# Kernel tuning notes

Measured on AMD Instinct MI355X. Metric: run time of the kernel, lower is better.

## Reference

```python
import jax, jax.numpy as jnp
import numpy as np

EPS = 1e-5

def rotate_half(x):
    # interleaved pairs: (..., d*2) -> stack(-x2, x1) interleaved back
    x = x.reshape(*x.shape[:-1], -1, 2)
    x1, x2 = x[..., 0], x[..., 1]
    return jnp.stack((-x2, x1), axis=-1).reshape(*x.shape[:-2], -1)

def apply_rotary(freqs, x):
    # freqs: (b, n, d); x: (b, h, n, d) -> broadcast over heads (unsqueeze at dim=1)
    f = freqs[:, None, :, :]
    return x * jnp.cos(f) + rotate_half(x) * jnp.sin(f)

def layer_norm(x, g, b):
    mu = jnp.mean(x, axis=-1, keepdims=True)
    var = jnp.var(x, axis=-1, keepdims=True)
    return (x - mu) * jax.lax.rsqrt(var + EPS) * g + b

def setup_inputs() -> dict:
    key = jax.random.key(0)
    ks = jax.random.split(key, 10)
    b, nq, nkv, dim, h, dh = 8, 1024, 2048, 512, 8, 64
    inner = h * dh
    return {
        "x_query": jax.random.normal(ks[0], (b, nq, dim), jnp.float32),
        "x_context": jax.random.normal(ks[1], (b, nkv, dim), jnp.float32),
        "rotary_time_emb_query": jax.random.normal(ks[2], (b, nq, dh), jnp.float32),
        "rotary_time_emb_context": jax.random.normal(ks[3], (b, nkv, dh), jnp.float32),
        "context_mask": jnp.ones((b, nkv), dtype=bool),
        "ln_q_g": jnp.ones((dim,), jnp.float32),
        "ln_q_b": jnp.zeros((dim,), jnp.float32),
        "ln_c_g": jnp.ones((dim,), jnp.float32),
        "ln_c_b": jnp.zeros((dim,), jnp.float32),
        "Wq": jax.random.normal(ks[4], (dim, inner), jnp.float32) * 0.02,
        "Wkv": jax.random.normal(ks[5], (dim, 2 * inner), jnp.float32) * 0.02,
        "Wo": jax.random.normal(ks[6], (inner, dim), jnp.float32) * 0.02,
        "bo": jnp.zeros((dim,), jnp.float32),
    }

def reference(x_query, x_context, rotary_time_emb_query, rotary_time_emb_context,
              context_mask, ln_q_g, ln_q_b, ln_c_g, ln_c_b, Wq, Wkv, Wo, bo):
    h = 8
    xq = layer_norm(x_query, ln_q_g, ln_q_b)
    xc = layer_norm(x_context, ln_c_g, ln_c_b)
    q = xq @ Wq                       # (b, nq, inner)
    kv = xc @ Wkv                     # (b, nkv, 2*inner)
    k, v = jnp.split(kv, 2, axis=-1)
    split_heads = lambda t: t.reshape(t.shape[0], t.shape[1], h, -1).transpose(0, 2, 1, 3)
    q, k, v = split_heads(q), split_heads(k), split_heads(v)  # (b, h, n, dh)
    q = apply_rotary(rotary_time_emb_query, q)
    k = apply_rotary(rotary_time_emb_context, k)
    v = apply_rotary(rotary_time_emb_context, v)   # rotate_value=True
    dh = q.shape[-1]
    scale = 1.0 / jnp.sqrt(jnp.float32(dh))
    scores = jnp.einsum('bhqd,bhkd->bhqk', q, k) * scale
    neg = jnp.finfo(scores.dtype).min
    scores = jnp.where(context_mask[:, None, None, :], scores, neg)
    attn = jax.nn.softmax(scores, axis=-1)
    out = jnp.einsum('bhqk,bhkd->bhqd', attn, v)
    out = apply_rotary(-rotary_time_emb_query, out)  # inverse rotation
    out = out.transpose(0, 2, 1, 3).reshape(out.shape[0], out.shape[2], -1)  # (b, nq, inner)
    return out @ Wo + bo
```

## Files before the change

kernel.cpp:

```cpp
#include <hip/hip_runtime.h>
#include <hip/hip_bf16.h>
#include <math.h>

#define BB 8
#define NQ 1024
#define NKV 2048
#define DIM 512
#define H 8
#define DH 64
#define INNER 512
#define SCALE_LOG2E 0.18033688011112042f

typedef __bf16 bf16x8 __attribute__((ext_vector_type(8)));
typedef float f32x4 __attribute__((ext_vector_type(4)));
typedef unsigned int u32x4 __attribute__((ext_vector_type(4)));

__device__ __forceinline__ unsigned short f2bf(float f) {
  union { float f; unsigned int u; } v; v.f = f;
  unsigned int r = v.u + 0x7fffu + ((v.u >> 16) & 1u);
  return (unsigned short)(r >> 16);
}
__device__ __forceinline__ float bf2f(unsigned short h) {
  union { unsigned int u; float f; } v; v.u = ((unsigned int)h) << 16;
  return v.f;
}

__device__ __forceinline__ void gl_lds16(const unsigned short* g, unsigned short* l) {
  __builtin_amdgcn_global_load_lds(
      (const __attribute__((address_space(1))) unsigned int*)g,
      (__attribute__((address_space(3))) unsigned int*)l, 16, 0, 0);
}

__global__ __launch_bounds__(256) void prep_weights(
    const float* __restrict__ Wq, const float* __restrict__ Wkv,
    const float* __restrict__ Wo,
    unsigned short* __restrict__ WqT, unsigned short* __restrict__ WkvT,
    unsigned short* __restrict__ WohT, unsigned short* __restrict__ WolT) {
  __shared__ float T[64][65];
  int blk = blockIdx.x;
  const float* src; int Wd, ti, tj, mode;
  unsigned short* dst = nullptr;
  if (blk < 64) { src = Wq;  dst = WqT;  Wd = 512;  ti = blk >> 3; tj = blk & 7; mode = 0; }
  else if (blk < 192) { int b2 = blk - 64; src = Wkv; dst = WkvT; Wd = 1024; ti = b2 >> 4; tj = b2 & 15; mode = 0; }
  else { int b2 = blk - 192; src = Wo; Wd = 512; ti = b2 >> 3; tj = b2 & 7; mode = 1; }
  int t = threadIdx.x;
#pragma unroll
  for (int i = 0; i < 16; ++i) {
    int idx = i * 256 + t;
    int r = idx >> 6, c = idx & 63;
    T[r][c] = src[(size_t)(ti * 64 + r) * Wd + tj * 64 + c];
  }
  __syncthreads();
#pragma unroll
  for (int i = 0; i < 16; ++i) {
    int idx = i * 256 + t;
    int n = idx >> 6, k = idx & 63;
    float v = T[k][n];
    size_t off = (size_t)(tj * 64 + n) * 512 + ti * 64 + k;
    if (mode == 0) {
      dst[off] = f2bf(v);
    } else {
      unsigned short hb = f2bf(v);
      WohT[off] = hb;
      WolT[off] = f2bf(v - bf2f(hb));
    }
  }
}

__global__ __launch_bounds__(256) void ln_kernel(
    const float* __restrict__ xq, const float* __restrict__ xc,
    const float* __restrict__ gq, const float* __restrict__ bq,
    const float* __restrict__ gc, const float* __restrict__ bc,
    unsigned short* __restrict__ xq_bf, unsigned short* __restrict__ xc_bf) {
  int row = blockIdx.x;
  const float* x; const float* g; const float* bb; unsigned short* out;
  if (row < BB * NQ) {
    x = xq + (size_t)row * DIM; g = gq; bb = bq; out = xq_bf + (size_t)row * DIM;
  } else {
    int r = row - BB * NQ;
    x = xc + (size_t)r * DIM; g = gc; bb = bc; out = xc_bf + (size_t)r * DIM;
  }
  int t = threadIdx.x;
  float2 v = *reinterpret_cast<const float2*>(x + t * 2);
  float s = v.x + v.y;
  float ss = v.x * v.x + v.y * v.y;
#pragma unroll
  for (int d = 1; d < 64; d <<= 1) { s += __shfl_xor(s, d); ss += __shfl_xor(ss, d); }
  __shared__ float red[8];
  int wid = t >> 6, lane = t & 63;
  if (lane == 0) { red[wid] = s; red[4 + wid] = ss; }
  __syncthreads();
  s = red[0] + red[1] + red[2] + red[3];
  ss = red[4] + red[5] + red[6] + red[7];
  float mu = s * (1.0f / DIM);
  float var = ss * (1.0f / DIM) - mu * mu;
  float rs = rsqrtf(var + 1e-5f);
  float y0 = (v.x - mu) * rs * g[t * 2] + bb[t * 2];
  float y1 = (v.y - mu) * rs * g[t * 2 + 1] + bb[t * 2 + 1];
  ushort2 o; o.x = f2bf(y0); o.y = f2bf(y1);
  *reinterpret_cast<ushort2*>(out + t * 2) = o;
}

__device__ __forceinline__ void gemm128_mainloop(
    const unsigned short* __restrict__ A, const unsigned short* __restrict__ WT,
    unsigned short* As, unsigned short* Ws,
    int rowBase, int colBase, f32x4 acc[4][4]) {
  const int t = threadIdx.x;
  const int w = t >> 6, l = t & 63;
  const int l15 = l & 15, lg = l >> 4, c7 = l15 & 7;
  const int wr = w >> 1, wc = w & 1;
  const int lrow = l >> 3;
  const int lchunk = (l & 7) ^ lrow;
  const int frag = (lg ^ c7) * 8;
  const unsigned short* Ag = A + (size_t)rowBase * 512;
  const unsigned short* Wg = WT + (size_t)colBase * 512;
#pragma unroll
  for (int m = 0; m < 4; ++m)
#pragma unroll
    for (int n = 0; n < 4; ++n) acc[m][n] = f32x4{0.f, 0.f, 0.f, 0.f};
  for (int kb = 0; kb < 512; kb += 64) {
#pragma unroll
    for (int i = 0; i < 4; ++i) {
      const int seg = w * 4 + i;
      const size_t goff = (size_t)(seg * 8 + lrow) * 512 + kb + lchunk * 8;
      gl_lds16(Ag + goff, As + seg * 512);
      gl_lds16(Wg + goff, Ws + seg * 512);
    }
    __syncthreads();
#pragma unroll
    for (int ks = 0; ks < 2; ++ks) {
      const int xo = ks ? 32 : 0;
      bf16x8 af[4], bf_[4];
#pragma unroll
      for (int m = 0; m < 4; ++m)
        af[m] = *reinterpret_cast<const bf16x8*>(
            &As[(wr * 64 + m * 16 + l15) * 64 + (frag ^ xo)]);
#pragma unroll
      for (int n = 0; n < 4; ++n)
        bf_[n] = *reinterpret_cast<const bf16x8*>(
            &Ws[(wc * 64 + n * 16 + l15) * 64 + (frag ^ xo)]);
#pragma unroll
      for (int m = 0; m < 4; ++m)
#pragma unroll
        for (int n = 0; n < 4; ++n)
          acc[m][n] = __builtin_amdgcn_mfma_f32_16x16x32_bf16(af[m], bf_[n], acc[m][n], 0, 0, 0);
    }
    __syncthreads();
  }
}

__global__ __launch_bounds__(256) void proj_q(
    const unsigned short* __restrict__ xq_bf, const unsigned short* __restrict__ WqT,
    const float* __restrict__ rotq, unsigned short* __restrict__ Qb) {
  __shared__ __align__(16) char smem[128 * 66 * 4];
  unsigned short* As = (unsigned short*)smem;
  unsigned short* Ws = (unsigned short*)(smem + 16384);
  float (*Cs)[66] = (float(*)[66])smem;
  int o = blockIdx.x;
  int swz = ((o & 7) << 5) | (o >> 3);
  int bn = swz & 3, bm = swz >> 2;
  f32x4 acc[4][4];
  gemm128_mainloop(xq_bf, WqT, As, Ws, bm * 128, bn * 128, acc);
  const int t = threadIdx.x;
  const int w = t >> 6, l = t & 63;
  const int l15 = l & 15, lg = l >> 4;
  const int wr = w >> 1, wc = w & 1;
#pragma unroll
  for (int hc = 0; hc < 2; ++hc) {
    if (wc == hc) {
#pragma unroll
      for (int m = 0; m < 4; ++m)
#pragma unroll
        for (int n = 0; n < 4; ++n)
#pragma unroll
          for (int r = 0; r < 4; ++r)
            Cs[wr * 64 + m * 16 + lg * 4 + r][n * 16 + l15] = acc[m][n][r];
    }
    __syncthreads();
    const int head = bn * 2 + hc;
#pragma unroll
    for (int i = 0; i < 16; ++i) {
      int p = i * 256 + t;
      int row = p >> 5, pc = p & 31, d0 = pc * 2;
      int grow = bm * 128 + row;
      float c0 = Cs[row][d0], c1 = Cs[row][d0 + 1];
      const float* f = rotq + (size_t)grow * DH + d0;
      float f0 = f[0], f1 = f[1], s0, s1, co0, co1;
      __sincosf(f0, &s0, &co0);
      __sincosf(f1, &s1, &co1);
      float o0 = (c0 * co0 - c1 * s0) * SCALE_LOG2E;
      float o1 = (c1 * co1 + c0 * s1) * SCALE_LOG2E;
      ushort2 ov; ov.x = f2bf(o0); ov.y = f2bf(o1);
      int b = grow >> 10, qq = grow & 1023;
      *reinterpret_cast<ushort2*>(Qb + (((size_t)(b * H + head) * NQ + qq) * DH + d0)) = ov;
    }
    __syncthreads();
  }
}

__global__ __launch_bounds__(256) void proj_kv(
    const unsigned short* __restrict__ xc_bf, const unsigned short* __restrict__ WkvT,
    const float* __restrict__ rotc, const int* __restrict__ cmask,
    unsigned short* __restrict__ Kb, unsigned short* __restrict__ VTb) {
  __shared__ __align__(16) char smem[128 * 66 * 4];
  unsigned short* As = (unsigned short*)smem;
  unsigned short* Ws = (unsigned short*)(smem + 16384);
  float (*Cs)[66] = (float(*)[66])smem;
  int o = blockIdx.x;
  int swz = ((o & 7) << 7) | (o >> 3);
  int bn = swz & 7, bm = swz >> 3;
  f32x4 acc[4][4];
  gemm128_mainloop(xc_bf, WkvT, As, Ws, bm * 128, bn * 128, acc);
  const int t = threadIdx.x;
  const int w = t >> 6, l = t & 63;
  const int l15 = l & 15, lg = l >> 4;
  const int wr = w >> 1, wc = w & 1;
#pragma unroll
  for (int hc = 0; hc < 2; ++hc) {
    if (wc == hc) {
#pragma unroll
      for (int m = 0; m < 4; ++m)
#pragma unroll
        for (int n = 0; n < 4; ++n)
#pragma unroll
          for (int r = 0; r < 4; ++r)
            Cs[wr * 64 + m * 16 + lg * 4 + r][n * 16 + l15] = acc[m][n][r];
    }
    __syncthreads();
    const int g = bn * 2 + hc;
    const int h = g & 7;
    if (g < 8) {
#pragma unroll
      for (int i = 0; i < 16; ++i) {
        int p = i * 256 + t;
        int row = p >> 5, pc = p & 31, d0 = pc * 2;
        int grow = bm * 128 + row;
        float c0 = Cs[row][d0], c1 = Cs[row][d0 + 1];
        const float* f = rotc + (size_t)grow * DH + d0;
        float f0 = f[0], f1 = f[1], s0, s1, co0, co1;
        __sincosf(f0, &s0, &co0);
        __sincosf(f1, &s1, &co1);
        float mf = cmask[grow] ? 1.f : 0.f;
        float o0 = (c0 * co0 - c1 * s0) * mf;
        float o1 = (c1 * co1 + c0 * s1) * mf;
        int b = grow >> 11, kk = grow & 2047;
        ushort2 ov; ov.x = f2bf(o0); ov.y = f2bf(o1);
        *reinterpret_cast<ushort2*>(Kb + (((size_t)(b * H + h) * NKV + kk) * DH + d0)) = ov;
      }
    } else {
      int oc = t & 7;
      int dd0 = t >> 3;
#pragma unroll
      for (int ch = 0; ch < 2; ++ch) {
        int ch64 = bm * 2 + ch;
        int bb = ch64 >> 5, chunk = ch64 & 31;
        unsigned short* vbase = VTb + (((size_t)(bb * H + h) * 32 + chunk) * 64) * 64;
#pragma unroll
        for (int half = 0; half < 2; ++half) {
          int d = dd0 + half * 32;
          u32x4 pack;
#pragma unroll
          for (int j2 = 0; j2 < 4; ++j2) {
            unsigned int lohi[2];
#pragma unroll
            for (int e = 0; e < 2; ++e) {
              int p = oc * 8 + j2 * 2 + e;
              int pp = p & 31;
              int kv = (p >> 5) * 32 + ((pp & 1) ? ((pp >> 1) + 16) : (pp >> 1));
              float c0 = Cs[ch * 64 + kv][d], cx = Cs[ch * 64 + kv][d ^ 1];
              float f = rotc[(size_t)(ch64 * 64 + kv) * DH + d];
              float sn, cs;
              __sincosf(f, &sn, &cs);
              float mf = cmask[ch64 * 64 + kv] ? 1.f : 0.f;
              float val = ((d & 1) ? (c0 * cs + cx * sn) : (c0 * cs - cx * sn)) * mf;
              lohi[e] = f2bf(val);
            }
            pack[j2] = lohi[0] | (lohi[1] << 16);
          }
          *reinterpret_cast<u32x4*>(vbase + d * 64 + oc * 8) = pack;
        }
      }
    }
    __syncthreads();
  }
}

__global__ __launch_bounds__(256) void attn_kernel(
    const unsigned short* __restrict__ Qb, const unsigned short* __restrict__ Kb,
    const unsigned short* __restrict__ VTb, const int* __restrict__ mask,
    const float* __restrict__ rotq,
    unsigned short* __restrict__ Ahb, unsigned short* __restrict__ Alb) {
  __shared__ unsigned short Ks[2 * 64 * 64];
  __shared__ unsigned short Vs[2 * 64 * 64];
  __shared__ unsigned short Ps[4 * 16 * 64];
  int ob = blockIdx.x;
  int swz = ((ob & 7) << 7) + (ob >> 3);
  int qb = swz & 15;
  int bh = swz >> 4;
  int b = bh >> 3, hh = bh & 7;
  int t = threadIdx.x, w = t >> 6, l = t & 63;
  int l15 = l & 15, lg = l >> 4;
  int c7 = l15 & 7;

  float nmasked;
  {
    const int* mrow = mask + b * NKV;
    float msum = 0.f;
#pragma unroll
    for (int i = 0; i < 8; ++i) {
      int4 m = *reinterpret_cast<const int4*>(mrow + l * 4 + i * 256);
      msum += (m.x ? 1.f : 0.f) + (m.y ? 1.f : 0.f) +
              (m.z ? 1.f : 0.f) + (m.w ? 1.f : 0.f);
    }
#pragma unroll
    for (int d = 1; d < 64; d <<= 1) msum += __shfl_xor(msum, d);
    nmasked = (float)NKV - msum;
  }

  const unsigned short* qrow = Qb + ((size_t)bh * NQ + qb * 64 + w * 16 + l15) * DH;
  bf16x8 qa0 = *reinterpret_cast<const bf16x8*>(qrow + lg * 8);
  bf16x8 qa1 = *reinterpret_cast<const bf16x8*>(qrow + 32 + lg * 8);

  float plsum[4] = {0.f, 0.f, 0.f, 0.f};
  f32x4 acc[4];
#pragma unroll
  for (int ct = 0; ct < 4; ++ct) acc[ct] = f32x4{0.f, 0.f, 0.f, 0.f};

  const int srow = t >> 2;
  const int sseg = (t & 3) * 16;
  const int sdst0 = srow * 64 + ((2 * (t & 3)) ^ (srow & 7)) * 8;
  const int frag = (lg ^ c7) * 8;
  const int kbase = l15 * 64 + frag;
  const int prbase = w * 1024 + l15 * 64 + frag;
  unsigned int* pw = reinterpret_cast<unsigned int*>(Ps);
  const int lg4 = lg * 4, l3 = l15 & 3, sD = l15 >> 2;

  const unsigned short* gk = Kb + ((size_t)bh * NKV + srow) * DH + sseg;
  const unsigned short* gv = VTb + (((size_t)bh * 32) * 64 + srow) * 64 + sseg;

  bf16x8 kr0 = *reinterpret_cast<const bf16x8*>(gk);
  bf16x8 kr1 = *reinterpret_cast<const bf16x8*>(gk + 8);
  bf16x8 vr0 = *reinterpret_cast<const bf16x8*>(gv);
  bf16x8 vr1 = *reinterpret_cast<const bf16x8*>(gv + 8);
  gk += 4096; gv += 4096;

#pragma unroll 2
  for (int ic = 0; ic < NKV / 64; ++ic) {
    const int bo_ = (ic & 1) << 12;
    *reinterpret_cast<bf16x8*>(&Ks[bo_ + sdst0])       = kr0;
    *reinterpret_cast<bf16x8*>(&Ks[bo_ + (sdst0 ^ 8)]) = kr1;
    *reinterpret_cast<bf16x8*>(&Vs[bo_ + sdst0])       = vr0;
    *reinterpret_cast<bf16x8*>(&Vs[bo_ + (sdst0 ^ 8)]) = vr1;
    __syncthreads();
    if (ic + 1 < NKV / 64) {
      kr0 = *reinterpret_cast<const bf16x8*>(gk);
      kr1 = *reinterpret_cast<const bf16x8*>(gk + 8);
      vr0 = *reinterpret_cast<const bf16x8*>(gv);
      vr1 = *reinterpret_cast<const bf16x8*>(gv + 8);
      gk += 4096; gv += 4096;
    }
    f32x4 s[4];
    __builtin_amdgcn_s_setprio(1);
#pragma unroll
    for (int tt = 0; tt < 4; ++tt) {
      f32x4 z = f32x4{0.f, 0.f, 0.f, 0.f};
      bf16x8 k0 = *reinterpret_cast<const bf16x8*>(&Ks[bo_ + tt * 1024 + kbase]);
      z = __builtin_amdgcn_mfma_f32_16x16x32_bf16(qa0, k0, z, 0, 0, 0);
      bf16x8 k1 = *reinterpret_cast<const bf16x8*>(&Ks[bo_ + tt * 1024 + (kbase ^ 32)]);
      z = __builtin_amdgcn_mfma_f32_16x16x32_bf16(qa1, k1, z, 0, 0, 0);
      s[tt] = z;
    }
    __builtin_amdgcn_s_setprio(0);
    float p[4][4];
#pragma unroll
    for (int tt = 0; tt < 4; ++tt)
#pragma unroll
      for (int r = 0; r < 4; ++r) {
        float e;
        asm("v_exp_f32 %0, %1" : "=v"(e) : "v"(s[tt][r]));
        p[tt][r] = e;
      }
#pragma unroll
    for (int r = 0; r < 4; ++r)
      plsum[r] += (p[0][r] + p[1][r]) + (p[2][r] + p[3][r]);
#pragma unroll
    for (int r = 0; r < 4; ++r) {
      unsigned int d01, d23;
      asm("v_cvt_pk_bf16_f32 %0, %1, %2" : "=v"(d01) : "v"(p[0][r]), "v"(p[1][r]));
      asm("v_cvt_pk_bf16_f32 %0, %1, %2" : "=v"(d23) : "v"(p[2][r]), "v"(p[3][r]));
      int row = lg4 + r;
      int rb = row & 7;
      int dwl = ((sD ^ rb) << 2) + l3;
      int pb = w * 512 + row * 32 + dwl;
      pw[pb] = d01;
      pw[pb ^ 16] = d23;
    }
    asm volatile("s_waitcnt lgkmcnt(0)" ::: "memory");
    __builtin_amdgcn_sched_barrier(0);
    __builtin_amdgcn_s_setprio(1);
#pragma unroll
    for (int ks = 0; ks < 2; ++ks) {
      bf16x8 pa = *reinterpret_cast<const bf16x8*>(&Ps[(prbase ^ (ks ? 32 : 0))]);
#pragma unroll
      for (int ct = 0; ct < 4; ++ct) {
        bf16x8 vb = *reinterpret_cast<const bf16x8*>(
            &Vs[bo_ + ct * 1024 + (kbase ^ (ks ? 32 : 0))]);
        acc[ct] = __builtin_amdgcn_mfma_f32_16x16x32_bf16(pa, vb, acc[ct], 0, 0, 0);
      }
    }
    __builtin_amdgcn_s_setprio(0);
  }
#pragma unroll
  for (int d = 1; d < 16; d <<= 1)
#pragma unroll
    for (int r = 0; r < 4; ++r) plsum[r] += __shfl_xor(plsum[r], d);
  float inv[4];
#pragma unroll
  for (int r = 0; r < 4; ++r) inv[r] = 1.0f / (plsum[r] - nmasked);

  int q0 = qb * 64 + w * 16 + lg * 4;
#pragma unroll
  for (int r = 0; r < 4; ++r) {
    int grow = b * NQ + q0 + r;
    const float* frow = rotq + (size_t)grow * DH;
    size_t obase = (size_t)grow * INNER + hh * DH;
#pragma unroll
    for (int ct = 0; ct < 4; ++ct) {
      int d = ct * 16 + l15;
      float x = acc[ct][r] * inv[r];
      float nb = __shfl_xor(x, 1);
      float f = frow[d];
      float sn, cs;
      __sincosf(f, &sn, &cs);
      float ov = (d & 1) ? (x * cs - nb * sn) : (x * cs + nb * sn);
      unsigned short hb = f2bf(ov);
      Ahb[obase + d] = hb;
      Alb[obase + d] = f2bf(ov - bf2f(hb));
    }
  }
}

__global__ __launch_bounds__(256) void final_gemm(
    const unsigned short* __restrict__ Ah, const unsigned short* __restrict__ Al,
    const unsigned short* __restrict__ Wh, const unsigned short* __restrict__ Wl,
    const float* __restrict__ bo, float* __restrict__ out) {
  __shared__ __align__(16) char smem[65536];
  unsigned short* AhS = (unsigned short*)smem;
  unsigned short* AlS = (unsigned short*)(smem + 16384);
  unsigned short* WhS = (unsigned short*)(smem + 32768);
  unsigned short* WlS = (unsigned short*)(smem + 49152);
  int o = blockIdx.x;
  int swz = ((o & 7) << 5) | (o >> 3);
  int bn = swz & 3, bm = swz >> 2;
  const int t = threadIdx.x;
  const int w = t >> 6, l = t & 63;
  const int l15 = l & 15, lg = l >> 4, c7 = l15 & 7;
  const int wr = w >> 1, wc = w & 1;
  const int lrow = l >> 3;
  const int lchunk = (l & 7) ^ lrow;
  const int frag = (lg ^ c7) * 8;
  const unsigned short* Agh = Ah + (size_t)bm * 128 * 512;
  const unsigned short* Agl = Al + (size_t)bm * 128 * 512;
  const unsigned short* Wgh = Wh + (size_t)bn * 128 * 512;
  const unsigned short* Wgl = Wl + (size_t)bn * 128 * 512;
  f32x4 acc[4][4];
#pragma unroll
  for (int m = 0; m < 4; ++m)
#pragma unroll
    for (int n = 0; n < 4; ++n) acc[m][n] = f32x4{0.f, 0.f, 0.f, 0.f};
  for (int kb = 0; kb < 512; kb += 64) {
#pragma unroll
    for (int i = 0; i < 4; ++i) {
      const int seg = w * 4 + i;
      const size_t goff = (size_t)(seg * 8 + lrow) * 512 + kb + lchunk * 8;
      gl_lds16(Agh + goff, AhS + seg * 512);
      gl_lds16(Agl + goff, AlS + seg * 512);
      gl_lds16(Wgh + goff, WhS + seg * 512);
      gl_lds16(Wgl + goff, WlS + seg * 512);
    }
    __syncthreads();
#pragma unroll
    for (int ks = 0; ks < 2; ++ks) {
      const int xo = ks ? 32 : 0;
      bf16x8 ah[4], al[4], wh[4], wl[4];
#pragma unroll
      for (int m = 0; m < 4; ++m) {
        const int off = (wr * 64 + m * 16 + l15) * 64 + (frag ^ xo);
        ah[m] = *reinterpret_cast<const bf16x8*>(&AhS[off]);
        al[m] = *reinterpret_cast<const bf16x8*>(&AlS[off]);
      }
#pragma unroll
      for (int n = 0; n < 4; ++n) {
        const int off = (wc * 64 + n * 16 + l15) * 64 + (frag ^ xo);
        wh[n] = *reinterpret_cast<const bf16x8*>(&WhS[off]);
        wl[n] = *reinterpret_cast<const bf16x8*>(&WlS[off]);
      }
#pragma unroll
      for (int m = 0; m < 4; ++m)
#pragma unroll
        for (int n = 0; n < 4; ++n) {
          acc[m][n] = __builtin_amdgcn_mfma_f32_16x16x32_bf16(ah[m], wh[n], acc[m][n], 0, 0, 0);
          acc[m][n] = __builtin_amdgcn_mfma_f32_16x16x32_bf16(al[m], wh[n], acc[m][n], 0, 0, 0);
          acc[m][n] = __builtin_amdgcn_mfma_f32_16x16x32_bf16(ah[m], wl[n], acc[m][n], 0, 0, 0);
        }
    }
    __syncthreads();
  }
  const int row0 = bm * 128 + wr * 64;
  const int col0 = bn * 128 + wc * 64;
#pragma unroll
  for (int m = 0; m < 4; ++m)
#pragma unroll
    for (int n = 0; n < 4; ++n) {
      int col = col0 + n * 16 + l15;
      float bv = bo[col];
#pragma unroll
      for (int r = 0; r < 4; ++r)
        out[(size_t)(row0 + m * 16 + lg * 4 + r) * 512 + col] = acc[m][n][r] + bv;
    }
}

extern "C" void kernel_launch(void* const* d_in, const int* in_sizes, int n_in,
                              void* d_out, int out_size, void* d_ws, size_t ws_size,
                              hipStream_t stream) {
  const float* x_query   = (const float*)d_in[0];
  const float* x_context = (const float*)d_in[1];
  const float* rot_q     = (const float*)d_in[2];
  const float* rot_c     = (const float*)d_in[3];
  const int*   cmask     = (const int*)d_in[4];
  const float* ln_q_g    = (const float*)d_in[5];
  const float* ln_q_b    = (const float*)d_in[6];
  const float* ln_c_g    = (const float*)d_in[7];
  const float* ln_c_b    = (const float*)d_in[8];
  const float* Wq        = (const float*)d_in[9];
  const float* Wkv       = (const float*)d_in[10];
  const float* Wo        = (const float*)d_in[11];
  const float* bo        = (const float*)d_in[12];
  float* out = (float*)d_out;

  char* ws = (char*)d_ws;
  unsigned short* xq_bf = (unsigned short*)(ws + 0);
  unsigned short* xc_bf = (unsigned short*)(ws + 8388608);
  unsigned short* Ahb   = (unsigned short*)(ws + 0);
  unsigned short* Alb   = (unsigned short*)(ws + 8388608);
  unsigned short* WqT   = (unsigned short*)(ws + 25165824);
  unsigned short* WkvT  = (unsigned short*)(ws + 25690112);
  unsigned short* Qb    = (unsigned short*)(ws + 26738688);
  unsigned short* Kb    = (unsigned short*)(ws + 35127296);
  unsigned short* VTb   = (unsigned short*)(ws + 51904512);
  unsigned short* WohT  = (unsigned short*)(ws + 68681728);
  unsigned short* WolT  = (unsigned short*)(ws + 69206016);

  prep_weights<<<dim3(256), dim3(256), 0, stream>>>(Wq, Wkv, Wo, WqT, WkvT, WohT, WolT);
  ln_kernel<<<dim3(24576), dim3(256), 0, stream>>>(x_query, x_context, ln_q_g, ln_q_b,
                                                   ln_c_g, ln_c_b, xq_bf, xc_bf);
  proj_q<<<dim3(256), dim3(256), 0, stream>>>(xq_bf, WqT, rot_q, Qb);
  proj_kv<<<dim3(1024), dim3(256), 0, stream>>>(xc_bf, WkvT, rot_c, cmask, Kb, VTb);
  attn_kernel<<<dim3(1024), dim3(256), 0, stream>>>(Qb, Kb, VTb, cmask, rot_q, Ahb, Alb);
  final_gemm<<<dim3(256), dim3(256), 0, stream>>>(Ahb, Alb, WohT, WolT, bo, out);
}
```

Baseline: 158.3 us.

## Merge prep and layernorm launches, fuse Q/KV projections, shrink final GEMM tile

Weight preparation and layernorm now run in one kernel, with each layernorm block handling 12 rows. The Q and KV projection kernels are merged into a single launch that branches on block index. The final output GEMM tile shrinks from 128x128 to 128x64, doubling the grid to 512 blocks and reducing LDS use. The aim is to cut launch count and tail idle time and to raise occupancy, at the cost of more redundant A-tile loads in the final GEMM and an extra barrier per layernorm row.

```diff
diff --git a/kernel.cpp b/kernel.cpp
--- a/kernel.cpp
+++ b/kernel.cpp
@@ -31,74 +31,77 @@
       (__attribute__((address_space(3))) unsigned int*)l, 16, 0, 0);
 }
 
-__global__ __launch_bounds__(256) void prep_weights(
+__global__ __launch_bounds__(256) void prep_ln(
     const float* __restrict__ Wq, const float* __restrict__ Wkv,
     const float* __restrict__ Wo,
     unsigned short* __restrict__ WqT, unsigned short* __restrict__ WkvT,
-    unsigned short* __restrict__ WohT, unsigned short* __restrict__ WolT) {
-  __shared__ float T[64][65];
-  int blk = blockIdx.x;
-  const float* src; int Wd, ti, tj, mode;
-  unsigned short* dst = nullptr;
-  if (blk < 64) { src = Wq;  dst = WqT;  Wd = 512;  ti = blk >> 3; tj = blk & 7; mode = 0; }
-  else if (blk < 192) { int b2 = blk - 64; src = Wkv; dst = WkvT; Wd = 1024; ti = b2 >> 4; tj = b2 & 15; mode = 0; }
-  else { int b2 = blk - 192; src = Wo; Wd = 512; ti = b2 >> 3; tj = b2 & 7; mode = 1; }
-  int t = threadIdx.x;
-#pragma unroll
-  for (int i = 0; i < 16; ++i) {
-    int idx = i * 256 + t;
-    int r = idx >> 6, c = idx & 63;
-    T[r][c] = src[(size_t)(ti * 64 + r) * Wd + tj * 64 + c];
-  }
-  __syncthreads();
-#pragma unroll
-  for (int i = 0; i < 16; ++i) {
-    int idx = i * 256 + t;
-    int n = idx >> 6, k = idx & 63;
-    float v = T[k][n];
-    size_t off = (size_t)(tj * 64 + n) * 512 + ti * 64 + k;
-    if (mode == 0) {
-      dst[off] = f2bf(v);
-    } else {
-      unsigned short hb = f2bf(v);
-      WohT[off] = hb;
-      WolT[off] = f2bf(v - bf2f(hb));
-    }
-  }
-}
-
-__global__ __launch_bounds__(256) void ln_kernel(
+    unsigned short* __restrict__ WohT, unsigned short* __restrict__ WolT,
     const float* __restrict__ xq, const float* __restrict__ xc,
     const float* __restrict__ gq, const float* __restrict__ bq,
     const float* __restrict__ gc, const float* __restrict__ bc,
     unsigned short* __restrict__ xq_bf, unsigned short* __restrict__ xc_bf) {
-  int row = blockIdx.x;
-  const float* x; const float* g; const float* bb; unsigned short* out;
-  if (row < BB * NQ) {
-    x = xq + (size_t)row * DIM; g = gq; bb = bq; out = xq_bf + (size_t)row * DIM;
+  __shared__ float T[64][65];
+  __shared__ float red[8];
+  int blk = blockIdx.x;
+  int t = threadIdx.x;
+  if (blk < 2048) {
+    int wid = t >> 6, lane = t & 63;
+    for (int rr = 0; rr < 12; ++rr) {
+      int row = blk * 12 + rr;
+      const float* x; const float* g; const float* bbv; unsigned short* outp;
+      if (row < BB * NQ) {
+        x = xq + (size_t)row * DIM; g = gq; bbv = bq; outp = xq_bf + (size_t)row * DIM;
+      } else {
+        int r2 = row - BB * NQ;
+        x = xc + (size_t)r2 * DIM; g = gc; bbv = bc; outp = xc_bf + (size_t)r2 * DIM;
+      }
+      float2 v = *reinterpret_cast<const float2*>(x + t * 2);
+      float s = v.x + v.y;
+      float ss = v.x * v.x + v.y * v.y;
+#pragma unroll
+      for (int d = 1; d < 64; d <<= 1) { s += __shfl_xor(s, d); ss += __shfl_xor(ss, d); }
+      if (lane == 0) { red[wid] = s; red[4 + wid] = ss; }
+      __syncthreads();
+      s = red[0] + red[1] + red[2] + red[3];
+      ss = red[4] + red[5] + red[6] + red[7];
+      __syncthreads();
+      float mu = s * (1.0f / DIM);
+      float var = ss * (1.0f / DIM) - mu * mu;
+      float rs = rsqrtf(var + 1e-5f);
+      float y0 = (v.x - mu) * rs * g[t * 2] + bbv[t * 2];
+      float y1 = (v.y - mu) * rs * g[t * 2 + 1] + bbv[t * 2 + 1];
+      ushort2 o; o.x = f2bf(y0); o.y = f2bf(y1);
+      *reinterpret_cast<ushort2*>(outp + t * 2) = o;
+    }
   } else {
-    int r = row - BB * NQ;
-    x = xc + (size_t)r * DIM; g = gc; bb = bc; out = xc_bf + (size_t)r * DIM;
-  }
-  int t = threadIdx.x;
-  float2 v = *reinterpret_cast<const float2*>(x + t * 2);
-  float s = v.x + v.y;
-  float ss = v.x * v.x + v.y * v.y;
-#pragma unroll
-  for (int d = 1; d < 64; d <<= 1) { s += __shfl_xor(s, d); ss += __shfl_xor(ss, d); }
-  __shared__ float red[8];
-  int wid = t >> 6, lane = t & 63;
-  if (lane == 0) { red[wid] = s; red[4 + wid] = ss; }
-  __syncthreads();
-  s = red[0] + red[1] + red[2] + red[3];
-  ss = red[4] + red[5] + red[6] + red[7];
-  float mu = s * (1.0f / DIM);
-  float var = ss * (1.0f / DIM) - mu * mu;
-  float rs = rsqrtf(var + 1e-5f);
-  float y0 = (v.x - mu) * rs * g[t * 2] + bb[t * 2];
-  float y1 = (v.y - mu) * rs * g[t * 2 + 1] + bb[t * 2 + 1];
-  ushort2 o; o.x = f2bf(y0); o.y = f2bf(y1);
-  *reinterpret_cast<ushort2*>(out + t * 2) = o;
+    int blk2 = blk - 2048;
+    const float* src; int Wd, ti, tj, mode;
+    unsigned short* dst = nullptr;
+    if (blk2 < 64) { src = Wq;  dst = WqT;  Wd = 512;  ti = blk2 >> 3; tj = blk2 & 7; mode = 0; }
+    else if (blk2 < 192) { int b2 = blk2 - 64; src = Wkv; dst = WkvT; Wd = 1024; ti = b2 >> 4; tj = b2 & 15; mode = 0; }
+    else { int b2 = blk2 - 192; src = Wo; Wd = 512; ti = b2 >> 3; tj = b2 & 7; mode = 1; }
+#pragma unroll
+    for (int i = 0; i < 16; ++i) {
+      int idx = i * 256 + t;
+      int r = idx >> 6, c = idx & 63;
+      T[r][c] = src[(size_t)(ti * 64 + r) * Wd + tj * 64 + c];
+    }
+    __syncthreads();
+#pragma unroll
+    for (int i = 0; i < 16; ++i) {
+      int idx = i * 256 + t;
+      int n = idx >> 6, k = idx & 63;
+      float v = T[k][n];
+      size_t off = (size_t)(tj * 64 + n) * 512 + ti * 64 + k;
+      if (mode == 0) {
+        dst[off] = f2bf(v);
+      } else {
+        unsigned short hb = f2bf(v);
+        WohT[off] = hb;
+        WolT[off] = f2bf(v - bf2f(hb));
+      }
+    }
+  }
 }
 
 __device__ __forceinline__ void gemm128_mainloop(
@@ -149,139 +152,131 @@
   }
 }
 
-__global__ __launch_bounds__(256) void proj_q(
-    const unsigned short* __restrict__ xq_bf, const unsigned short* __restrict__ WqT,
-    const float* __restrict__ rotq, unsigned short* __restrict__ Qb) {
+__global__ __launch_bounds__(256) void proj_fused(
+    const unsigned short* __restrict__ xq_bf, const unsigned short* __restrict__ xc_bf,
+    const unsigned short* __restrict__ WqT, const unsigned short* __restrict__ WkvT,
+    const float* __restrict__ rotq, const float* __restrict__ rotc,
+    const int* __restrict__ cmask,
+    unsigned short* __restrict__ Qb, unsigned short* __restrict__ Kb,
+    unsigned short* __restrict__ VTb) {
   __shared__ __align__(16) char smem[128 * 66 * 4];
   unsigned short* As = (unsigned short*)smem;
   unsigned short* Ws = (unsigned short*)(smem + 16384);
   float (*Cs)[66] = (float(*)[66])smem;
-  int o = blockIdx.x;
-  int swz = ((o & 7) << 5) | (o >> 3);
-  int bn = swz & 3, bm = swz >> 2;
-  f32x4 acc[4][4];
-  gemm128_mainloop(xq_bf, WqT, As, Ws, bm * 128, bn * 128, acc);
   const int t = threadIdx.x;
   const int w = t >> 6, l = t & 63;
   const int l15 = l & 15, lg = l >> 4;
   const int wr = w >> 1, wc = w & 1;
-#pragma unroll
-  for (int hc = 0; hc < 2; ++hc) {
-    if (wc == hc) {
-#pragma unroll
-      for (int m = 0; m < 4; ++m)
-#pragma unroll
-        for (int n = 0; n < 4; ++n)
-#pragma unroll
-          for (int r = 0; r < 4; ++r)
-            Cs[wr * 64 + m * 16 + lg * 4 + r][n * 16 + l15] = acc[m][n][r];
-    }
-    __syncthreads();
-    const int head = bn * 2 + hc;
-#pragma unroll
-    for (int i = 0; i < 16; ++i) {
-      int p = i * 256 + t;
-      int row = p >> 5, pc = p & 31, d0 = pc * 2;
-      int grow = bm * 128 + row;
-      float c0 = Cs[row][d0], c1 = Cs[row][d0 + 1];
-      const float* f = rotq + (size_t)grow * DH + d0;
-      float f0 = f[0], f1 = f[1], s0, s1, co0, co1;
-      __sincosf(f0, &s0, &co0);
-      __sincosf(f1, &s1, &co1);
-      float o0 = (c0 * co0 - c1 * s0) * SCALE_LOG2E;
-      float o1 = (c1 * co1 + c0 * s1) * SCALE_LOG2E;
-      ushort2 ov; ov.x = f2bf(o0); ov.y = f2bf(o1);
-      int b = grow >> 10, qq = grow & 1023;
-      *reinterpret_cast<ushort2*>(Qb + (((size_t)(b * H + head) * NQ + qq) * DH + d0)) = ov;
-    }
-    __syncthreads();
-  }
-}
-
-__global__ __launch_bounds__(256) void proj_kv(
-    const unsigned short* __restrict__ xc_bf, const unsigned short* __restrict__ WkvT,
-    const float* __restrict__ rotc, const int* __restrict__ cmask,
-    unsigned short* __restrict__ Kb, unsigned short* __restrict__ VTb) {
-  __shared__ __align__(16) char smem[128 * 66 * 4];
-  unsigned short* As = (unsigned short*)smem;
-  unsigned short* Ws = (unsigned short*)(smem + 16384);
-  float (*Cs)[66] = (float(*)[66])smem;
+  f32x4 acc[4][4];
   int o = blockIdx.x;
-  int swz = ((o & 7) << 7) | (o >> 3);
-  int bn = swz & 7, bm = swz >> 3;
-  f32x4 acc[4][4];
-  gemm128_mainloop(xc_bf, WkvT, As, Ws, bm * 128, bn * 128, acc);
-  const int t = threadIdx.x;
-  const int w = t >> 6, l = t & 63;
-  const int l15 = l & 15, lg = l >> 4;
-  const int wr = w >> 1, wc = w & 1;
-#pragma unroll
-  for (int hc = 0; hc < 2; ++hc) {
-    if (wc == hc) {
-#pragma unroll
-      for (int m = 0; m < 4; ++m)
-#pragma unroll
-        for (int n = 0; n < 4; ++n)
-#pragma unroll
-          for (int r = 0; r < 4; ++r)
-            Cs[wr * 64 + m * 16 + lg * 4 + r][n * 16 + l15] = acc[m][n][r];
-    }
-    __syncthreads();
-    const int g = bn * 2 + hc;
-    const int h = g & 7;
-    if (g < 8) {
+  if (o < 1024) {
+    int swz = ((o & 7) << 7) | (o >> 3);
+    int bn = swz & 7, bm = swz >> 3;
+    gemm128_mainloop(xc_bf, WkvT, As, Ws, bm * 128, bn * 128, acc);
+#pragma unroll
+    for (int hc = 0; hc < 2; ++hc) {
+      if (wc == hc) {
+#pragma unroll
+        for (int m = 0; m < 4; ++m)
+#pragma unroll
+          for (int n = 0; n < 4; ++n)
+#pragma unroll
+            for (int r = 0; r < 4; ++r)
+              Cs[wr * 64 + m * 16 + lg * 4 + r][n * 16 + l15] = acc[m][n][r];
+      }
+      __syncthreads();
+      const int g = bn * 2 + hc;
+      const int h = g & 7;
+      if (g < 8) {
+#pragma unroll
+        for (int i = 0; i < 16; ++i) {
+          int p = i * 256 + t;
+          int row = p >> 5, pc = p & 31, d0 = pc * 2;
+          int grow = bm * 128 + row;
+          float c0 = Cs[row][d0], c1 = Cs[row][d0 + 1];
+          const float* f = rotc + (size_t)grow * DH + d0;
+          float f0 = f[0], f1 = f[1], s0, s1, co0, co1;
+          __sincosf(f0, &s0, &co0);
+          __sincosf(f1, &s1, &co1);
+          float mf = cmask[grow] ? 1.f : 0.f;
+          float o0 = (c0 * co0 - c1 * s0) * mf;
+          float o1 = (c1 * co1 + c0 * s1) * mf;
+          int b = grow >> 11, kk = grow & 2047;
+          ushort2 ov; ov.x = f2bf(o0); ov.y = f2bf(o1);
+          *reinterpret_cast<ushort2*>(Kb + (((size_t)(b * H + h) * NKV + kk) * DH + d0)) = ov;
+        }
+      } else {
+        int oc = t & 7;
+        int dd0 = t >> 3;
+#pragma unroll
+        for (int ch = 0; ch < 2; ++ch) {
+          int ch64 = bm * 2 + ch;
+          int bb = ch64 >> 5, chunk = ch64 & 31;
+          unsigned short* vbase = VTb + (((size_t)(bb * H + h) * 32 + chunk) * 64) * 64;
+#pragma unroll
+          for (int half = 0; half < 2; ++half) {
+            int d = dd0 + half * 32;
+            u32x4 pack;
+#pragma unroll
+            for (int j2 = 0; j2 < 4; ++j2) {
+              unsigned int lohi[2];
+#pragma unroll
+              for (int e = 0; e < 2; ++e) {
+                int p = oc * 8 + j2 * 2 + e;
+                int pp = p & 31;
+                int kv = (p >> 5) * 32 + ((pp & 1) ? ((pp >> 1) + 16) : (pp >> 1));
+                float c0 = Cs[ch * 64 + kv][d], cx = Cs[ch * 64 + kv][d ^ 1];
+                float f = rotc[(size_t)(ch64 * 64 + kv) * DH + d];
+                float sn, cs;
+                __sincosf(f, &sn, &cs);
+                float mf = cmask[ch64 * 64 + kv] ? 1.f : 0.f;
+                float val = ((d & 1) ? (c0 * cs + cx * sn) : (c0 * cs - cx * sn)) * mf;
+                lohi[e] = f2bf(val);
+              }
+              pack[j2] = lohi[0] | (lohi[1] << 16);
+            }
+            *reinterpret_cast<u32x4*>(vbase + d * 64 + oc * 8) = pack;
+          }
+        }
+      }
+      __syncthreads();
+    }
+  } else {
+    int o2 = o - 1024;
+    int swz = ((o2 & 7) << 5) | (o2 >> 3);
+    int bn = swz & 3, bm = swz >> 2;
+    gemm128_mainloop(xq_bf, WqT, As, Ws, bm * 128, bn * 128, acc);
+#pragma unroll
+    for (int hc = 0; hc < 2; ++hc) {
+      if (wc == hc) {
+#pragma unroll
+        for (int m = 0; m < 4; ++m)
+#pragma unroll
+          for (int n = 0; n < 4; ++n)
+#pragma unroll
+            for (int r = 0; r < 4; ++r)
+              Cs[wr * 64 + m * 16 + lg * 4 + r][n * 16 + l15] = acc[m][n][r];
+      }
+      __syncthreads();
+      const int head = bn * 2 + hc;
 #pragma unroll
       for (int i = 0; i < 16; ++i) {
         int p = i * 256 + t;
         int row = p >> 5, pc = p & 31, d0 = pc * 2;
         int grow = bm * 128 + row;
         float c0 = Cs[row][d0], c1 = Cs[row][d0 + 1];
-        const float* f = rotc + (size_t)grow * DH + d0;
+        const float* f = rotq + (size_t)grow * DH + d0;
         float f0 = f[0], f1 = f[1], s0, s1, co0, co1;
         __sincosf(f0, &s0, &co0);
         __sincosf(f1, &s1, &co1);
-        float mf = cmask[grow] ? 1.f : 0.f;
-        float o0 = (c0 * co0 - c1 * s0) * mf;
-        float o1 = (c1 * co1 + c0 * s1) * mf;
-        int b = grow >> 11, kk = grow & 2047;
+        float o0 = (c0 * co0 - c1 * s0) * SCALE_LOG2E;
+        float o1 = (c1 * co1 + c0 * s1) * SCALE_LOG2E;
         ushort2 ov; ov.x = f2bf(o0); ov.y = f2bf(o1);
-        *reinterpret_cast<ushort2*>(Kb + (((size_t)(b * H + h) * NKV + kk) * DH + d0)) = ov;
-      }
-    } else {
-      int oc = t & 7;
-      int dd0 = t >> 3;
-#pragma unroll
-      for (int ch = 0; ch < 2; ++ch) {
-        int ch64 = bm * 2 + ch;
-        int bb = ch64 >> 5, chunk = ch64 & 31;
-        unsigned short* vbase = VTb + (((size_t)(bb * H + h) * 32 + chunk) * 64) * 64;
-#pragma unroll
-        for (int half = 0; half < 2; ++half) {
-          int d = dd0 + half * 32;
-          u32x4 pack;
-#pragma unroll
-          for (int j2 = 0; j2 < 4; ++j2) {
-            unsigned int lohi[2];
-#pragma unroll
-            for (int e = 0; e < 2; ++e) {
-              int p = oc * 8 + j2 * 2 + e;
-              int pp = p & 31;
-              int kv = (p >> 5) * 32 + ((pp & 1) ? ((pp >> 1) + 16) : (pp >> 1));
-              float c0 = Cs[ch * 64 + kv][d], cx = Cs[ch * 64 + kv][d ^ 1];
-              float f = rotc[(size_t)(ch64 * 64 + kv) * DH + d];
-              float sn, cs;
-              __sincosf(f, &sn, &cs);
-              float mf = cmask[ch64 * 64 + kv] ? 1.f : 0.f;
-              float val = ((d & 1) ? (c0 * cs + cx * sn) : (c0 * cs - cx * sn)) * mf;
-              lohi[e] = f2bf(val);
-            }
-            pack[j2] = lohi[0] | (lohi[1] << 16);
-          }
-          *reinterpret_cast<u32x4*>(vbase + d * 64 + oc * 8) = pack;
-        }
-      }
-    }
-    __syncthreads();
+        int b = grow >> 10, qq = grow & 1023;
+        *reinterpret_cast<ushort2*>(Qb + (((size_t)(b * H + head) * NQ + qq) * DH + d0)) = ov;
+      }
+      __syncthreads();
+    }
   }
 }
 
@@ -444,14 +439,14 @@
     const unsigned short* __restrict__ Ah, const unsigned short* __restrict__ Al,
     const unsigned short* __restrict__ Wh, const unsigned short* __restrict__ Wl,
     const float* __restrict__ bo, float* __restrict__ out) {
-  __shared__ __align__(16) char smem[65536];
+  __shared__ __align__(16) char smem[49152];
   unsigned short* AhS = (unsigned short*)smem;
   unsigned short* AlS = (unsigned short*)(smem + 16384);
   unsigned short* WhS = (unsigned short*)(smem + 32768);
-  unsigned short* WlS = (unsigned short*)(smem + 49152);
+  unsigned short* WlS = (unsigned short*)(smem + 40960);
   int o = blockIdx.x;
-  int swz = ((o & 7) << 5) | (o >> 3);
-  int bn = swz & 3, bm = swz >> 2;
+  int swz = ((o & 7) << 6) | (o >> 3);
+  int bn = swz & 7, bm = swz >> 3;
   const int t = threadIdx.x;
   const int w = t >> 6, l = t & 63;
   const int l15 = l & 15, lg = l >> 4, c7 = l15 & 7;
@@ -461,13 +456,13 @@
   const int frag = (lg ^ c7) * 8;
   const unsigned short* Agh = Ah + (size_t)bm * 128 * 512;
   const unsigned short* Agl = Al + (size_t)bm * 128 * 512;
-  const unsigned short* Wgh = Wh + (size_t)bn * 128 * 512;
-  const unsigned short* Wgl = Wl + (size_t)bn * 128 * 512;
-  f32x4 acc[4][4];
+  const unsigned short* Wgh = Wh + (size_t)bn * 64 * 512;
+  const unsigned short* Wgl = Wl + (size_t)bn * 64 * 512;
+  f32x4 acc[4][2];
 #pragma unroll
   for (int m = 0; m < 4; ++m)
 #pragma unroll
-    for (int n = 0; n < 4; ++n) acc[m][n] = f32x4{0.f, 0.f, 0.f, 0.f};
+    for (int n = 0; n < 2; ++n) acc[m][n] = f32x4{0.f, 0.f, 0.f, 0.f};
   for (int kb = 0; kb < 512; kb += 64) {
 #pragma unroll
     for (int i = 0; i < 4; ++i) {
@@ -475,6 +470,11 @@
       const size_t goff = (size_t)(seg * 8 + lrow) * 512 + kb + lchunk * 8;
       gl_lds16(Agh + goff, AhS + seg * 512);
       gl_lds16(Agl + goff, AlS + seg * 512);
+    }
+#pragma unroll
+    for (int i = 0; i < 2; ++i) {
+      const int seg = w * 2 + i;
+      const size_t goff = (size_t)(seg * 8 + lrow) * 512 + kb + lchunk * 8;
       gl_lds16(Wgh + goff, WhS + seg * 512);
       gl_lds16(Wgl + goff, WlS + seg * 512);
     }
@@ -482,7 +482,7 @@
 #pragma unroll
     for (int ks = 0; ks < 2; ++ks) {
       const int xo = ks ? 32 : 0;
-      bf16x8 ah[4], al[4], wh[4], wl[4];
+      bf16x8 ah[4], al[4], wh[2], wl[2];
 #pragma unroll
       for (int m = 0; m < 4; ++m) {
         const int off = (wr * 64 + m * 16 + l15) * 64 + (frag ^ xo);
@@ -490,15 +490,15 @@
         al[m] = *reinterpret_cast<const bf16x8*>(&AlS[off]);
       }
 #pragma unroll
-      for (int n = 0; n < 4; ++n) {
-        const int off = (wc * 64 + n * 16 + l15) * 64 + (frag ^ xo);
+      for (int n = 0; n < 2; ++n) {
+        const int off = (wc * 32 + n * 16 + l15) * 64 + (frag ^ xo);
         wh[n] = *reinterpret_cast<const bf16x8*>(&WhS[off]);
         wl[n] = *reinterpret_cast<const bf16x8*>(&WlS[off]);
       }
 #pragma unroll
       for (int m = 0; m < 4; ++m)
 #pragma unroll
-        for (int n = 0; n < 4; ++n) {
+        for (int n = 0; n < 2; ++n) {
           acc[m][n] = __builtin_amdgcn_mfma_f32_16x16x32_bf16(ah[m], wh[n], acc[m][n], 0, 0, 0);
           acc[m][n] = __builtin_amdgcn_mfma_f32_16x16x32_bf16(al[m], wh[n], acc[m][n], 0, 0, 0);
           acc[m][n] = __builtin_amdgcn_mfma_f32_16x16x32_bf16(ah[m], wl[n], acc[m][n], 0, 0, 0);
@@ -507,11 +507,11 @@
     __syncthreads();
   }
   const int row0 = bm * 128 + wr * 64;
-  const int col0 = bn * 128 + wc * 64;
+  const int col0 = bn * 64 + wc * 32;
 #pragma unroll
   for (int m = 0; m < 4; ++m)
 #pragma unroll
-    for (int n = 0; n < 4; ++n) {
+    for (int n = 0; n < 2; ++n) {
       int col = col0 + n * 16 + l15;
       float bv = bo[col];
 #pragma unroll
@@ -551,11 +551,11 @@
   unsigned short* WohT  = (unsigned short*)(ws + 68681728);
   unsigned short* WolT  = (unsigned short*)(ws + 69206016);
 
-  prep_weights<<<dim3(256), dim3(256), 0, stream>>>(Wq, Wkv, Wo, WqT, WkvT, WohT, WolT);
-  ln_kernel<<<dim3(24576), dim3(256), 0, stream>>>(x_query, x_context, ln_q_g, ln_q_b,
-                                                   ln_c_g, ln_c_b, xq_bf, xc_bf);
-  proj_q<<<dim3(256), dim3(256), 0, stream>>>(xq_bf, WqT, rot_q, Qb);
-  proj_kv<<<dim3(1024), dim3(256), 0, stream>>>(xc_bf, WkvT, rot_c, cmask, Kb, VTb);
+  prep_ln<<<dim3(2304), dim3(256), 0, stream>>>(
+      Wq, Wkv, Wo, WqT, WkvT, WohT, WolT,
+      x_query, x_context, ln_q_g, ln_q_b, ln_c_g, ln_c_b, xq_bf, xc_bf);
+  proj_fused<<<dim3(1280), dim3(256), 0, stream>>>(
+      xq_bf, xc_bf, WqT, WkvT, rot_q, rot_c, cmask, Qb, Kb, VTb);
   attn_kernel<<<dim3(1024), dim3(256), 0, stream>>>(Qb, Kb, VTb, cmask, rot_q, Ahb, Alb);
-  final_gemm<<<dim3(256), dim3(256), 0, stream>>>(Ahb, Alb, WohT, WolT, bo, out);
-}
+  final_gemm<<<dim3(512), dim3(256), 0, stream>>>(Ahb, Alb, WohT, WolT, bo, out);
+}
```

Result: faster. 146.4 us (-7.5%).
